# Kernel tuning notes

Hardware: AMD Instinct MI355X
Metric: run time of the kernel (lower is better)

The kernel has to match this reference:

```python
import jax, jax.numpy as jnp
import numpy as np

L, D, H, d = 16, 1024, 16, 64
NB, BS = 1024, 16        # num physical blocks, block size (tokens per block)
START_POS = 16368        # T = START_POS + L = 16384
SCALE = 1.0 / np.sqrt(d)


def setup_inputs() -> dict:
    key = jax.random.key(0)
    ks = jax.random.split(key, 5)
    return {
        "x": jax.random.normal(ks[0], (L, D), jnp.float32),
        "k_pool": jax.random.normal(ks[1], (NB, BS, H, d), jnp.float32),
        "v_pool": jax.random.normal(ks[2], (NB, BS, H, d), jnp.float32),
        "W_attn": jax.random.normal(ks[3], (D, 3 * D), jnp.float32) * 0.02,
        "b_attn": jnp.zeros((3 * D,), jnp.float32),
        "W_proj": jax.random.normal(ks[4], (D, D), jnp.float32) * 0.02,
        "b_proj": jnp.zeros((D,), jnp.float32),
        "block_ids": jnp.arange(NB, dtype=jnp.int64),
        "start_pos": START_POS,
    }


def reference(x, k_pool, v_pool, W_attn, b_attn, W_proj, b_proj, block_ids, start_pos):
    # QKV projection
    qkv = x @ W_attn + b_attn                      # [L, 3D]
    q, k, v = jnp.split(qkv, 3, axis=-1)
    q = q.reshape(L, H, d)
    k = k.reshape(L, H, d)
    v = v.reshape(L, H, d)

    # paged write of new K/V into the pool
    pos = start_pos + jnp.arange(L)                # logical positions of new tokens
    blk = block_ids[pos // BS]                     # physical block per token
    off = pos % BS
    k_pool = k_pool.at[blk, off].set(k)
    v_pool = v_pool.at[blk, off].set(v)

    # paged read of the full prefix [0, T)
    T = start_pos + L
    k_pos = jnp.arange(T)
    kb = block_ids[k_pos // BS]
    ko = k_pos % BS
    k_cache = k_pool[kb, ko]                       # [T, H, d]
    v_cache = v_pool[kb, ko]                       # [T, H, d]

    # attention: scores [H, L, T]
    scores = jnp.einsum("lhd,thd->hlt", q, k_cache) * SCALE
    mask = k_pos[None, :] > pos[:, None]           # [L, T] future positions
    scores = jnp.where(mask[None, :, :], -jnp.inf, scores)
    attn = jax.nn.softmax(scores.astype(jnp.float32), axis=-1).astype(scores.dtype)

    out = jnp.einsum("hlt,thd->lhd", attn, v_cache).reshape(L, D)
    return out @ W_proj + b_proj
```

## Files before the change

### kernel.cpp

```cpp
#include <hip/hip_runtime.h>
#include <math.h>

#define L_TOK 16
#define DMODEL 1024
#define NHEAD 16
#define DHEAD 64
#define NBLK 1024
#define BSZ 16
#define START_POS_C 16368
#define TTOT 16384
#define SPLITS 128
#define KSPLIT 16
#define QSCALE (0.125f * 1.4426950408889634f)

#define OFF_QKVP 0
#define OFF_QW   (OFF_QKVP + KSPLIT * L_TOK * 3 * DMODEL)
#define OFF_ACC  (OFF_QW + NHEAD * L_TOK * DHEAD)
#define OFF_M    (OFF_ACC + NHEAD * SPLITS * L_TOK * DHEAD)
#define OFF_SE   (OFF_M + NHEAD * SPLITS * L_TOK)
#define OFF_ATTN (OFF_SE + NHEAD * SPLITS * L_TOK)
#define OFF_PROJP (OFF_ATTN + L_TOK * DMODEL)
#define OFF_KNEW (OFF_PROJP + KSPLIT * L_TOK * DMODEL)
#define OFF_VNEW (OFF_KNEW + L_TOK * NHEAD * DHEAD)

typedef _Float16 half4_t __attribute__((ext_vector_type(4)));
typedef _Float16 half8_t __attribute__((ext_vector_type(8)));
typedef float float4v __attribute__((ext_vector_type(4)));

union H8 { _Float16 h[8]; half8_t v; };
union H4 { _Float16 h[4]; half4_t v; };

#define LDS_DMA16(gsrc, ldst)                                                        \
    __builtin_amdgcn_global_load_lds(                                                \
        (const __attribute__((address_space(1))) void*)(gsrc),                       \
        (__attribute__((address_space(3))) void*)(ldst), 16, 0, 0)

__device__ __forceinline__ void load_batch(float* buf, const float* Wp, int bk, int ncols) {
#pragma unroll
    for (int i = 0; i < 16; ++i) buf[i] = Wp[(size_t)(bk + i) * ncols];
}

__device__ __forceinline__ void fma_batch(float4v* acc_, const float* buf,
                                          const float* sxT, int bk) {
#pragma unroll
    for (int i = 0; i < 16; ++i) {
        const float wv_ = buf[i];
        const float4v* xp = (const float4v*)&sxT[(bk + i) * 20];
        float4v xa = xp[0], xb = xp[1], xc = xp[2], xd = xp[3];
        acc_[0] += xa * wv_;
        acc_[1] += xb * wv_;
        acc_[2] += xc * wv_;
        acc_[3] += xd * wv_;
    }
}

__global__ __launch_bounds__(256) void gemm_part(const float* __restrict__ x,
                                                 const float* __restrict__ W,
                                                 float* __restrict__ part,
                                                 int ncols) {
    const int col = blockIdx.x * 256 + threadIdx.x;
    const int k0 = blockIdx.y * (DMODEL / KSPLIT);

    __shared__ __align__(16) float sxT[64 * 20];
#pragma unroll
    for (int i = threadIdx.x; i < 64 * 16; i += 256) {
        int k = i & 63, l = i >> 6;
        sxT[k * 20 + l] = x[(size_t)l * DMODEL + k0 + k];
    }

    const float* Wp = W + (size_t)k0 * ncols + col;
    float wa[16], wb[16];
    load_batch(wa, Wp, 0, ncols);
    load_batch(wb, Wp, 16, ncols);
    __builtin_amdgcn_sched_barrier(0);
    __syncthreads();

    float4v acc_[4];
#pragma unroll
    for (int g = 0; g < 4; ++g) acc_[g] = (float4v){0.f, 0.f, 0.f, 0.f};

    fma_batch(acc_, wa, sxT, 0);
    load_batch(wa, Wp, 32, ncols);
    __builtin_amdgcn_sched_barrier(0);
    fma_batch(acc_, wb, sxT, 16);
    load_batch(wb, Wp, 48, ncols);
    __builtin_amdgcn_sched_barrier(0);
    fma_batch(acc_, wa, sxT, 32);
    fma_batch(acc_, wb, sxT, 48);

    const size_t base = ((size_t)blockIdx.y * L_TOK) * ncols + col;
#pragma unroll
    for (int g = 0; g < 4; ++g)
#pragma unroll
        for (int j = 0; j < 4; ++j)
            part[base + (size_t)(4 * g + j) * ncols] = acc_[g][j];
}

__global__ __launch_bounds__(256) void qkv_reduce_scatter(const float* __restrict__ part,
                                                          const float* __restrict__ b_attn,
                                                          float* __restrict__ qws,
                                                          float* __restrict__ knew,
                                                          float* __restrict__ vnew) {
    int tid = blockIdx.x * 256 + threadIdx.x;
    int n = tid % (3 * DMODEL);
    int l = tid / (3 * DMODEL);
    float p[KSPLIT];
#pragma unroll
    for (int kb = 0; kb < KSPLIT; ++kb)
        p[kb] = part[((size_t)kb * L_TOK + l) * (3 * DMODEL) + n];
    float s = b_attn[n];
#pragma unroll
    for (int st = 1; st < KSPLIT; st <<= 1)
#pragma unroll
        for (int i = 0; i < KSPLIT; i += 2 * st) p[i] += p[i + st];
    s += p[0];
    int sec = n >> 10;
    int m = n & (DMODEL - 1);
    int h = m >> 6;
    int dd = m & 63;
    if (sec == 0) {
        qws[(h * L_TOK + l) * DHEAD + dd] = s * QSCALE;
    } else {
        size_t idx = ((size_t)l * NHEAD + h) * DHEAD + dd;
        if (sec == 1) knew[idx] = s;
        else          vnew[idx] = s;
    }
}

__device__ __forceinline__ void stage_tile(const float* __restrict__ gk,
                                           const float* __restrict__ gv,
                                           float* kb, float* vb,
                                           int w, int lane, int hgrp) {
#pragma unroll
    for (int i = 0; i < 4; ++i) {
        const int tok = 4 * w + i;
        const int lx = lane ^ (tok & 7);
#pragma unroll
        for (int part = 0; part < 2; ++part) {
            const size_t go = (size_t)tok * 1024 + hgrp * 512 + part * 256 + lx * 4;
            LDS_DMA16(gk + go, kb + tok * 512 + part * 256);
            LDS_DMA16(gv + go, vb + tok * 512 + part * 256);
        }
    }
}

__device__ __forceinline__ void kv_base(const float* __restrict__ kpool,
                                        const float* __restrict__ vpool,
                                        const float* __restrict__ knew,
                                        const float* __restrict__ vnew,
                                        const int* blks, int s, int t,
                                        const float*& gk, const float*& gv) {
    if (s == SPLITS - 1 && t == 7) {
        gk = knew; gv = vnew;
    } else {
        gk = kpool + (size_t)blks[t] * 16384;
        gv = vpool + (size_t)blks[t] * 16384;
    }
}

__device__ __forceinline__ void attn_tile(const float* kt, const float* vt,
                                          int hh, half8_t qlo, half8_t qhi,
                                          float4v* acc, float& m_run, float& se_run,
                                          int tb, int c, int quad) {
    const int keyc = c & 7;
    const int hb = hh << 4;
    const float* krow = kt + c * 512;
    float4v a0 = *(const float4v*)&krow[(((hb | (2 * quad)) ^ keyc) << 2)];
    float4v a1 = *(const float4v*)&krow[(((hb | (2 * quad + 1)) ^ keyc) << 2)];
    float4v a2 = *(const float4v*)&krow[(((hb | (2 * quad + 8)) ^ keyc) << 2)];
    float4v a3 = *(const float4v*)&krow[(((hb | (2 * quad + 9)) ^ keyc) << 2)];
    H8 ka, kb;
    ka.h[0]=(_Float16)a0[0]; ka.h[1]=(_Float16)a0[1]; ka.h[2]=(_Float16)a0[2]; ka.h[3]=(_Float16)a0[3];
    ka.h[4]=(_Float16)a1[0]; ka.h[5]=(_Float16)a1[1]; ka.h[6]=(_Float16)a1[2]; ka.h[7]=(_Float16)a1[3];
    kb.h[0]=(_Float16)a2[0]; kb.h[1]=(_Float16)a2[1]; kb.h[2]=(_Float16)a2[2]; kb.h[3]=(_Float16)a2[3];
    kb.h[4]=(_Float16)a3[0]; kb.h[5]=(_Float16)a3[1]; kb.h[6]=(_Float16)a3[2]; kb.h[7]=(_Float16)a3[3];
    const float4v z4 = {0.f, 0.f, 0.f, 0.f};
    float4v st = __builtin_amdgcn_mfma_f32_16x16x32_f16(ka.v, qlo, z4, 0, 0, 0);
    st = __builtin_amdgcn_mfma_f32_16x16x32_f16(kb.v, qhi, st, 0, 0, 0);

    if (tb + 15 > START_POS_C) {
#pragma unroll
        for (int r = 0; r < 4; ++r)
            if (tb + 4 * quad + r > START_POS_C + c) st[r] = -INFINITY;
    }

    float tm = fmaxf(fmaxf(st[0], st[1]), fmaxf(st[2], st[3]));
    tm = fmaxf(tm, __shfl_xor(tm, 16, 64));
    tm = fmaxf(tm, __shfl_xor(tm, 32, 64));
    const float m_new = fmaxf(m_run, tm);
    const float fac = exp2f(m_run - m_new);
    H4 pa;
    pa.h[0]=(_Float16)exp2f(st[0]-m_new); pa.h[1]=(_Float16)exp2f(st[1]-m_new);
    pa.h[2]=(_Float16)exp2f(st[2]-m_new); pa.h[3]=(_Float16)exp2f(st[3]-m_new);
    float tsum = ((float)pa.h[0] + (float)pa.h[1]) + ((float)pa.h[2] + (float)pa.h[3]);
    tsum += __shfl_xor(tsum, 16, 64);
    tsum += __shfl_xor(tsum, 32, 64);
    se_run = se_run * fac + tsum;
    m_run = m_new;
    float4v fv;
    fv[0] = __shfl(fac, 4 * quad + 0, 64);
    fv[1] = __shfl(fac, 4 * quad + 1, 64);
    fv[2] = __shfl(fac, 4 * quad + 2, 64);
    fv[3] = __shfl(fac, 4 * quad + 3, 64);
#pragma unroll
    for (int ndv = 0; ndv < 4; ++ndv) acc[ndv] *= fv;
#pragma unroll
    for (int ndv = 0; ndv < 4; ++ndv) {
        H4 bf;
#pragma unroll
        for (int j = 0; j < 4; ++j) {
            const int tokr = 4 * quad + j;
            const int slot = (hb | (4 * ndv + (c >> 2))) ^ (tokr & 7);
            bf.h[j] = (_Float16)vt[tokr * 512 + (slot << 2) + (c & 3)];
        }
        acc[ndv] = __builtin_amdgcn_mfma_f32_16x16x16f16(pa.v, bf.v, acc[ndv], 0, 0, 0);
    }
}

__global__ __launch_bounds__(256, 1) void paged_attn(const float* __restrict__ kpool,
                                                     const float* __restrict__ vpool,
                                                     const int* __restrict__ block_ids,
                                                     const float* __restrict__ qws,
                                                     const float* __restrict__ knew,
                                                     const float* __restrict__ vnew,
                                                     float* __restrict__ accws,
                                                     float* __restrict__ m_arr,
                                                     float* __restrict__ se_arr) {
    const int hgrp = blockIdx.x;
    const int s = blockIdx.y;
    const int tid = threadIdx.x;
    const int w = tid >> 6;
    const int lane = tid & 63;
    const int c = lane & 15;
    const int quad = lane >> 4;

    __shared__ __align__(16) float kbuf[2][8192];
    __shared__ __align__(16) float vbuf[2][8192];

    int blks[8];
#pragma unroll
    for (int t = 0; t < 8; ++t) blks[t] = block_ids[s * 8 + t];

    const int h0 = hgrp * 8 + 2 * w;
    H8 qA0, qA1, qB0, qB1;
    {
        const float* qr = qws + ((size_t)(h0 * L_TOK + c)) * DHEAD + quad * 8;
        float4 x0 = *(const float4*)(qr),        x1 = *(const float4*)(qr + 4);
        float4 x2 = *(const float4*)(qr + 32),   x3 = *(const float4*)(qr + 36);
        float4 y0 = *(const float4*)(qr + 1024), y1 = *(const float4*)(qr + 1028);
        float4 y2 = *(const float4*)(qr + 1056), y3 = *(const float4*)(qr + 1060);
        qA0.h[0]=(_Float16)x0.x; qA0.h[1]=(_Float16)x0.y; qA0.h[2]=(_Float16)x0.z; qA0.h[3]=(_Float16)x0.w;
        qA0.h[4]=(_Float16)x1.x; qA0.h[5]=(_Float16)x1.y; qA0.h[6]=(_Float16)x1.z; qA0.h[7]=(_Float16)x1.w;
        qA1.h[0]=(_Float16)x2.x; qA1.h[1]=(_Float16)x2.y; qA1.h[2]=(_Float16)x2.z; qA1.h[3]=(_Float16)x2.w;
        qA1.h[4]=(_Float16)x3.x; qA1.h[5]=(_Float16)x3.y; qA1.h[6]=(_Float16)x3.z; qA1.h[7]=(_Float16)x3.w;
        qB0.h[0]=(_Float16)y0.x; qB0.h[1]=(_Float16)y0.y; qB0.h[2]=(_Float16)y0.z; qB0.h[3]=(_Float16)y0.w;
        qB0.h[4]=(_Float16)y1.x; qB0.h[5]=(_Float16)y1.y; qB0.h[6]=(_Float16)y1.z; qB0.h[7]=(_Float16)y1.w;
        qB1.h[0]=(_Float16)y2.x; qB1.h[1]=(_Float16)y2.y; qB1.h[2]=(_Float16)y2.z; qB1.h[3]=(_Float16)y2.w;
        qB1.h[4]=(_Float16)y3.x; qB1.h[5]=(_Float16)y3.y; qB1.h[6]=(_Float16)y3.z; qB1.h[7]=(_Float16)y3.w;
    }

    {
        const float* gk; const float* gv;
        kv_base(kpool, vpool, knew, vnew, blks, s, 0, gk, gv);
        stage_tile(gk, gv, kbuf[0], vbuf[0], w, lane, hgrp);
    }

    float4v accA[4], accB[4];
#pragma unroll
    for (int i = 0; i < 4; ++i) {
        accA[i] = (float4v){0.f, 0.f, 0.f, 0.f};
        accB[i] = (float4v){0.f, 0.f, 0.f, 0.f};
    }
    float mA = -INFINITY, seA = 0.f, mB = -INFINITY, seB = 0.f;

    float* kc = kbuf[0]; float* vc = vbuf[0];
    float* kn = kbuf[1]; float* vn = vbuf[1];

    for (int t = 0; t < 8; ++t) {
        if (t < 7) {
            const float* gk; const float* gv;
            kv_base(kpool, vpool, knew, vnew, blks, s, t + 1, gk, gv);
            stage_tile(gk, gv, kn, vn, w, lane, hgrp);
            asm volatile("s_waitcnt vmcnt(16)" ::: "memory");
        } else {
            asm volatile("s_waitcnt vmcnt(0)" ::: "memory");
        }
        __builtin_amdgcn_sched_barrier(0);
        __builtin_amdgcn_s_barrier();

        const int tb = s * 128 + t * 16;
        attn_tile(kc, vc, 2 * w,     qA0.v, qA1.v, accA, mA, seA, tb, c, quad);
        attn_tile(kc, vc, 2 * w + 1, qB0.v, qB1.v, accB, mB, seB, tb, c, quad);

        __builtin_amdgcn_s_barrier();
        float* tk = kc; kc = kn; kn = tk;
        float* tv = vc; vc = vn; vn = tv;
    }

    const size_t obA = ((size_t)(h0 * SPLITS + s) * L_TOK) * DHEAD;
    const size_t obB = ((size_t)((h0 + 1) * SPLITS + s) * L_TOK) * DHEAD;
#pragma unroll
    for (int ndv = 0; ndv < 4; ++ndv)
#pragma unroll
        for (int r = 0; r < 4; ++r) {
            accws[obA + (size_t)(4 * quad + r) * DHEAD + 16 * ndv + c] = accA[ndv][r];
            accws[obB + (size_t)(4 * quad + r) * DHEAD + 16 * ndv + c] = accB[ndv][r];
        }
    if (quad == 0) {
        const size_t mbA = (size_t)(h0 * SPLITS + s) * L_TOK + c;
        const size_t mbB = (size_t)((h0 + 1) * SPLITS + s) * L_TOK + c;
        m_arr[mbA] = mA; se_arr[mbA] = seA;
        m_arr[mbB] = mB; se_arr[mbB] = seB;
    }
}

__global__ __launch_bounds__(256) void combine(const float* __restrict__ accws,
                                               const float* __restrict__ m_arr,
                                               const float* __restrict__ se_arr,
                                               float* __restrict__ attnws) {
    const int h = blockIdx.x >> 4;
    const int l = blockIdx.x & 15;
    const int w = threadIdx.x >> 6;
    const int lane = threadIdx.x & 63;
    __shared__ float sm[4], sse[4], sacc[4][64];

    const size_t base = (size_t)h * SPLITS * L_TOK + l;

    float mreg[SPLITS / 4];
#pragma unroll
    for (int i = 0; i < SPLITS / 4; ++i)
        mreg[i] = m_arr[base + (size_t)(w + 4 * i) * L_TOK];
    float M = -INFINITY;
#pragma unroll
    for (int i = 0; i < SPLITS / 4; ++i) M = fmaxf(M, mreg[i]);

    float num = 0.f, den = 0.f;
#pragma unroll
    for (int i = 0; i < SPLITS / 4; ++i) {
        const size_t idx = base + (size_t)(w + 4 * i) * L_TOK;
        const float wgt = exp2f(mreg[i] - M);
        num = fmaf(wgt, accws[idx * DHEAD + lane], num);
        den = fmaf(wgt, se_arr[idx], den);
    }

    if (lane == 0) { sm[w] = M; sse[w] = den; }
    sacc[w][lane] = num;
    __syncthreads();
    if (w == 0) {
        const float M0 = fmaxf(fmaxf(sm[0], sm[1]), fmaxf(sm[2], sm[3]));
        float nn = 0.f, dd = 0.f;
#pragma unroll
        for (int i = 0; i < 4; ++i) {
            const float wgt = exp2f(sm[i] - M0);
            nn = fmaf(wgt, sacc[i][lane], nn);
            dd = fmaf(wgt, sse[i], dd);
        }
        attnws[(size_t)l * DMODEL + h * DHEAD + lane] = nn / dd;
    }
}

__global__ __launch_bounds__(256) void proj_reduce(const float* __restrict__ part,
                                                   const float* __restrict__ bias,
                                                   float* __restrict__ out) {
    int tid = blockIdx.x * 256 + threadIdx.x;
    int n = tid & (DMODEL - 1);
    int l = tid >> 10;
    float p[KSPLIT];
#pragma unroll
    for (int kb = 0; kb < KSPLIT; ++kb)
        p[kb] = part[((size_t)kb * L_TOK + l) * DMODEL + n];
#pragma unroll
    for (int st = 1; st < KSPLIT; st <<= 1)
#pragma unroll
        for (int i = 0; i < KSPLIT; i += 2 * st) p[i] += p[i + st];
    out[tid] = bias[n] + p[0];
}

extern "C" void kernel_launch(void* const* d_in, const int* in_sizes, int n_in,
                              void* d_out, int out_size, void* d_ws, size_t ws_size,
                              hipStream_t stream) {
    const float* x       = (const float*)d_in[0];
    const float* kpool   = (const float*)d_in[1];
    const float* vpool   = (const float*)d_in[2];
    const float* W_attn  = (const float*)d_in[3];
    const float* b_attn  = (const float*)d_in[4];
    const float* W_proj  = (const float*)d_in[5];
    const float* b_proj  = (const float*)d_in[6];
    const int* block_ids = (const int*)d_in[7];
    float* ws  = (float*)d_ws;
    float* out = (float*)d_out;

    gemm_part<<<dim3(12, KSPLIT), 256, 0, stream>>>(x, W_attn, ws + OFF_QKVP, 3 * DMODEL);
    qkv_reduce_scatter<<<192, 256, 0, stream>>>(ws + OFF_QKVP, b_attn,
                                                ws + OFF_QW, ws + OFF_KNEW, ws + OFF_VNEW);
    paged_attn<<<dim3(2, SPLITS), 256, 0, stream>>>(kpool, vpool, block_ids,
                                                    ws + OFF_QW, ws + OFF_KNEW, ws + OFF_VNEW,
                                                    ws + OFF_ACC, ws + OFF_M, ws + OFF_SE);
    combine<<<NHEAD * L_TOK, 256, 0, stream>>>(ws + OFF_ACC, ws + OFF_M, ws + OFF_SE,
                                               ws + OFF_ATTN);
    gemm_part<<<dim3(4, KSPLIT), 256, 0, stream>>>(ws + OFF_ATTN, W_proj, ws + OFF_PROJP, DMODEL);
    proj_reduce<<<64, 256, 0, stream>>>(ws + OFF_PROJP, b_proj, out);
}
```

Baseline: 199.2 us.

## Fuse all six stages into one cooperative persistent kernel with grid syncs

Merges the QKV GEMM, reduce/scatter, paged attention, combine, projection GEMM and final reduce into one cooperative kernel of 256 blocks, separated by grid-wide syncs. This removes five kernel launches and the gaps between them. In exchange every block reserves 128KB of LDS for all phases, and each grid sync costs something. The previous multi-kernel path stays as a fallback if the cooperative launch fails.

Result: slower. 351.7 us (+76.5%).

```diff
diff --git a/kernel.cpp b/kernel.cpp
--- a/kernel.cpp
+++ b/kernel.cpp
@@ -1,5 +1,8 @@
 #include <hip/hip_runtime.h>
+#include <hip/hip_cooperative_groups.h>
 #include <math.h>
+
+namespace cg = cooperative_groups;
 
 #define L_TOK 16
 #define DMODEL 1024
@@ -35,6 +38,7 @@
         (const __attribute__((address_space(1))) void*)(gsrc),                       \
         (__attribute__((address_space(3))) void*)(ldst), 16, 0, 0)
 
+
 __device__ __forceinline__ void load_batch(float* buf, const float* Wp, int bk, int ncols) {
 #pragma unroll
     for (int i = 0; i < 16; ++i) buf[i] = Wp[(size_t)(bk + i) * ncols];
@@ -54,31 +58,25 @@
     }
 }
 
-__global__ __launch_bounds__(256) void gemm_part(const float* __restrict__ x,
-                                                 const float* __restrict__ W,
-                                                 float* __restrict__ part,
-                                                 int ncols) {
-    const int col = blockIdx.x * 256 + threadIdx.x;
-    const int k0 = blockIdx.y * (DMODEL / KSPLIT);
-
-    __shared__ __align__(16) float sxT[64 * 20];
-#pragma unroll
-    for (int i = threadIdx.x; i < 64 * 16; i += 256) {
+__device__ __forceinline__ void gemm_body(const float* x, const float* W, float* part,
+                                          int ncols, int bx, int by, float* smem, int tid) {
+    const int col = bx * 256 + tid;
+    const int k0 = by * (DMODEL / KSPLIT);
+    float* sxT = smem;
+#pragma unroll
+    for (int i = tid; i < 64 * 16; i += 256) {
         int k = i & 63, l = i >> 6;
         sxT[k * 20 + l] = x[(size_t)l * DMODEL + k0 + k];
     }
-
     const float* Wp = W + (size_t)k0 * ncols + col;
     float wa[16], wb[16];
     load_batch(wa, Wp, 0, ncols);
     load_batch(wb, Wp, 16, ncols);
     __builtin_amdgcn_sched_barrier(0);
     __syncthreads();
-
     float4v acc_[4];
 #pragma unroll
     for (int g = 0; g < 4; ++g) acc_[g] = (float4v){0.f, 0.f, 0.f, 0.f};
-
     fma_batch(acc_, wa, sxT, 0);
     load_batch(wa, Wp, 32, ncols);
     __builtin_amdgcn_sched_barrier(0);
@@ -87,8 +85,7 @@
     __builtin_amdgcn_sched_barrier(0);
     fma_batch(acc_, wa, sxT, 32);
     fma_batch(acc_, wb, sxT, 48);
-
-    const size_t base = ((size_t)blockIdx.y * L_TOK) * ncols + col;
+    const size_t base = ((size_t)by * L_TOK) * ncols + col;
 #pragma unroll
     for (int g = 0; g < 4; ++g)
 #pragma unroll
@@ -96,14 +93,12 @@
             part[base + (size_t)(4 * g + j) * ncols] = acc_[g][j];
 }
 
-__global__ __launch_bounds__(256) void qkv_reduce_scatter(const float* __restrict__ part,
-                                                          const float* __restrict__ b_attn,
-                                                          float* __restrict__ qws,
-                                                          float* __restrict__ knew,
-                                                          float* __restrict__ vnew) {
-    int tid = blockIdx.x * 256 + threadIdx.x;
-    int n = tid % (3 * DMODEL);
-    int l = tid / (3 * DMODEL);
+__device__ __forceinline__ void qkv_reduce_body(const float* part, const float* b_attn,
+                                                float* qws, float* knew, float* vnew,
+                                                int b, int tid) {
+    int tg = b * 256 + tid;
+    int n = tg % (3 * DMODEL);
+    int l = tg / (3 * DMODEL);
     float p[KSPLIT];
 #pragma unroll
     for (int kb = 0; kb < KSPLIT; ++kb)
@@ -127,8 +122,7 @@
     }
 }
 
-__device__ __forceinline__ void stage_tile(const float* __restrict__ gk,
-                                           const float* __restrict__ gv,
+__device__ __forceinline__ void stage_tile(const float* gk, const float* gv,
                                            float* kb, float* vb,
                                            int w, int lane, int hgrp) {
 #pragma unroll
@@ -144,10 +138,8 @@
     }
 }
 
-__device__ __forceinline__ void kv_base(const float* __restrict__ kpool,
-                                        const float* __restrict__ vpool,
-                                        const float* __restrict__ knew,
-                                        const float* __restrict__ vnew,
+__device__ __forceinline__ void kv_base(const float* kpool, const float* vpool,
+                                        const float* knew, const float* vnew,
                                         const int* blks, int s, int t,
                                         const float*& gk, const float*& gv) {
     if (s == SPLITS - 1 && t == 7) {
@@ -217,25 +209,20 @@
     }
 }
 
-__global__ __launch_bounds__(256, 1) void paged_attn(const float* __restrict__ kpool,
-                                                     const float* __restrict__ vpool,
-                                                     const int* __restrict__ block_ids,
-                                                     const float* __restrict__ qws,
-                                                     const float* __restrict__ knew,
-                                                     const float* __restrict__ vnew,
-                                                     float* __restrict__ accws,
-                                                     float* __restrict__ m_arr,
-                                                     float* __restrict__ se_arr) {
-    const int hgrp = blockIdx.x;
-    const int s = blockIdx.y;
-    const int tid = threadIdx.x;
+__device__ __forceinline__ void attn_body(const float* kpool, const float* vpool,
+                                          const int* block_ids, const float* qws,
+                                          const float* knew, const float* vnew,
+                                          float* accws, float* m_arr, float* se_arr,
+                                          int hgrp, int s, int tid, float* smem) {
     const int w = tid >> 6;
     const int lane = tid & 63;
     const int c = lane & 15;
     const int quad = lane >> 4;
 
-    __shared__ __align__(16) float kbuf[2][8192];
-    __shared__ __align__(16) float vbuf[2][8192];
+    float* kb0 = smem;
+    float* kb1 = smem + 8192;
+    float* vb0 = smem + 16384;
+    float* vb1 = smem + 24576;
 
     int blks[8];
 #pragma unroll
@@ -262,7 +249,7 @@
     {
         const float* gk; const float* gv;
         kv_base(kpool, vpool, knew, vnew, blks, s, 0, gk, gv);
-        stage_tile(gk, gv, kbuf[0], vbuf[0], w, lane, hgrp);
+        stage_tile(gk, gv, kb0, vb0, w, lane, hgrp);
     }
 
     float4v accA[4], accB[4];
@@ -273,8 +260,8 @@
     }
     float mA = -INFINITY, seA = 0.f, mB = -INFINITY, seB = 0.f;
 
-    float* kc = kbuf[0]; float* vc = vbuf[0];
-    float* kn = kbuf[1]; float* vn = vbuf[1];
+    float* kc = kb0; float* vc = vb0;
+    float* kn = kb1; float* vn = vb1;
 
     for (int t = 0; t < 8; ++t) {
         if (t < 7) {
@@ -314,15 +301,14 @@
     }
 }
 
-__global__ __launch_bounds__(256) void combine(const float* __restrict__ accws,
-                                               const float* __restrict__ m_arr,
-                                               const float* __restrict__ se_arr,
-                                               float* __restrict__ attnws) {
-    const int h = blockIdx.x >> 4;
-    const int l = blockIdx.x & 15;
-    const int w = threadIdx.x >> 6;
-    const int lane = threadIdx.x & 63;
-    __shared__ float sm[4], sse[4], sacc[4][64];
+__device__ __forceinline__ void combine_body(const float* accws, const float* m_arr,
+                                             const float* se_arr, float* attnws,
+                                             int h, int l, int tid, float* smem) {
+    const int w = tid >> 6;
+    const int lane = tid & 63;
+    float* sm = smem;
+    float* sse = smem + 4;
+    float (*sacc)[64] = (float (*)[64])(smem + 8);
 
     const size_t base = (size_t)h * SPLITS * L_TOK + l;
 
@@ -359,12 +345,11 @@
     }
 }
 
-__global__ __launch_bounds__(256) void proj_reduce(const float* __restrict__ part,
-                                                   const float* __restrict__ bias,
-                                                   float* __restrict__ out) {
-    int tid = blockIdx.x * 256 + threadIdx.x;
-    int n = tid & (DMODEL - 1);
-    int l = tid >> 10;
+__device__ __forceinline__ void proj_reduce_body(const float* part, const float* bias,
+                                                 float* out, int b, int tid) {
+    int tg = b * 256 + tid;
+    int n = tg & (DMODEL - 1);
+    int l = tg >> 10;
     float p[KSPLIT];
 #pragma unroll
     for (int kb = 0; kb < KSPLIT; ++kb)
@@ -373,7 +358,85 @@
     for (int st = 1; st < KSPLIT; st <<= 1)
 #pragma unroll
         for (int i = 0; i < KSPLIT; i += 2 * st) p[i] += p[i + st];
-    out[tid] = bias[n] + p[0];
+    out[tg] = bias[n] + p[0];
+}
+
+__global__ __launch_bounds__(256, 1) void mega(const float* x, const float* kpool,
+                                               const float* vpool, const float* W_attn,
+                                               const float* b_attn, const float* W_proj,
+                                               const float* b_proj, const int* block_ids,
+                                               float* ws, float* out) {
+    cg::grid_group gg = cg::this_grid();
+    const int b = blockIdx.x;
+    const int tid = threadIdx.x;
+    __shared__ __align__(16) float smem[32768];
+
+    float* const qkvp   = ws + OFF_QKVP;
+    float* const qws    = ws + OFF_QW;
+    float* const accws  = ws + OFF_ACC;
+    float* const m_arr  = ws + OFF_M;
+    float* const se_arr = ws + OFF_SE;
+    float* const attnws = ws + OFF_ATTN;
+    float* const projp  = ws + OFF_PROJP;
+    float* const knew   = ws + OFF_KNEW;
+    float* const vnew   = ws + OFF_VNEW;
+
+    if (b < 192) gemm_body(x, W_attn, qkvp, 3 * DMODEL, b % 12, b / 12, smem, tid);
+    gg.sync();
+    if (b < 192) qkv_reduce_body(qkvp, b_attn, qws, knew, vnew, b, tid);
+    gg.sync();
+    attn_body(kpool, vpool, block_ids, qws, knew, vnew, accws, m_arr, se_arr,
+              b & 1, b >> 1, tid, smem);
+    gg.sync();
+    combine_body(accws, m_arr, se_arr, attnws, b >> 4, b & 15, tid, smem);
+    gg.sync();
+    if (b < 64) gemm_body(attnws, W_proj, projp, DMODEL, b % 4, b / 4, smem, tid);
+    gg.sync();
+    if (b < 64) proj_reduce_body(projp, b_proj, out, b, tid);
+}
+
+__global__ __launch_bounds__(256) void gemm_part_k(const float* __restrict__ x,
+                                                   const float* __restrict__ W,
+                                                   float* __restrict__ part, int ncols) {
+    __shared__ __align__(16) float sxT[64 * 20];
+    gemm_body(x, W, part, ncols, blockIdx.x, blockIdx.y, sxT, threadIdx.x);
+}
+
+__global__ __launch_bounds__(256) void qkv_reduce_k(const float* __restrict__ part,
+                                                    const float* __restrict__ b_attn,
+                                                    float* __restrict__ qws,
+                                                    float* __restrict__ knew,
+                                                    float* __restrict__ vnew) {
+    qkv_reduce_body(part, b_attn, qws, knew, vnew, blockIdx.x, threadIdx.x);
+}
+
+__global__ __launch_bounds__(256, 1) void paged_attn_k(const float* __restrict__ kpool,
+                                                       const float* __restrict__ vpool,
+                                                       const int* __restrict__ block_ids,
+                                                       const float* __restrict__ qws,
+                                                       const float* __restrict__ knew,
+                                                       const float* __restrict__ vnew,
+                                                       float* __restrict__ accws,
+                                                       float* __restrict__ m_arr,
+                                                       float* __restrict__ se_arr) {
+    __shared__ __align__(16) float smem[32768];
+    attn_body(kpool, vpool, block_ids, qws, knew, vnew, accws, m_arr, se_arr,
+              blockIdx.x, blockIdx.y, threadIdx.x, smem);
+}
+
+__global__ __launch_bounds__(256) void combine_k(const float* __restrict__ accws,
+                                                 const float* __restrict__ m_arr,
+                                                 const float* __restrict__ se_arr,
+                                                 float* __restrict__ attnws) {
+    __shared__ float smem[264];
+    combine_body(accws, m_arr, se_arr, attnws, blockIdx.x >> 4, blockIdx.x & 15,
+                 threadIdx.x, smem);
+}
+
+__global__ __launch_bounds__(256) void proj_reduce_k(const float* __restrict__ part,
+                                                     const float* __restrict__ bias,
+                                                     float* __restrict__ out) {
+    proj_reduce_body(part, bias, out, blockIdx.x, threadIdx.x);
 }
 
 extern "C" void kernel_launch(void* const* d_in, const int* in_sizes, int n_in,
@@ -390,14 +453,23 @@
     float* ws  = (float*)d_ws;
     float* out = (float*)d_out;
 
-    gemm_part<<<dim3(12, KSPLIT), 256, 0, stream>>>(x, W_attn, ws + OFF_QKVP, 3 * DMODEL);
-    qkv_reduce_scatter<<<192, 256, 0, stream>>>(ws + OFF_QKVP, b_attn,
-                                                ws + OFF_QW, ws + OFF_KNEW, ws + OFF_VNEW);
-    paged_attn<<<dim3(2, SPLITS), 256, 0, stream>>>(kpool, vpool, block_ids,
-                                                    ws + OFF_QW, ws + OFF_KNEW, ws + OFF_VNEW,
-                                                    ws + OFF_ACC, ws + OFF_M, ws + OFF_SE);
-    combine<<<NHEAD * L_TOK, 256, 0, stream>>>(ws + OFF_ACC, ws + OFF_M, ws + OFF_SE,
-                                               ws + OFF_ATTN);
-    gemm_part<<<dim3(4, KSPLIT), 256, 0, stream>>>(ws + OFF_ATTN, W_proj, ws + OFF_PROJP, DMODEL);
-    proj_reduce<<<64, 256, 0, stream>>>(ws + OFF_PROJP, b_proj, out);
-}
+    void* args[] = { (void*)&x, (void*)&kpool, (void*)&vpool, (void*)&W_attn,
+                     (void*)&b_attn, (void*)&W_proj, (void*)&b_proj,
+                     (void*)&block_ids, (void*)&ws, (void*)&out };
+    hipError_t err = hipLaunchCooperativeKernel((const void*)mega, dim3(256), dim3(256),
+                                                args, 0, stream);
+    if (err != hipSuccess) {
+        gemm_part_k<<<dim3(12, KSPLIT), 256, 0, stream>>>(x, W_attn, ws + OFF_QKVP, 3 * DMODEL);
+        qkv_reduce_k<<<192, 256, 0, stream>>>(ws + OFF_QKVP, b_attn,
+                                              ws + OFF_QW, ws + OFF_KNEW, ws + OFF_VNEW);
+        paged_attn_k<<<dim3(2, SPLITS), 256, 0, stream>>>(kpool, vpool, block_ids,
+                                                          ws + OFF_QW, ws + OFF_KNEW,
+                                                          ws + OFF_VNEW, ws + OFF_ACC,
+                                                          ws + OFF_M, ws + OFF_SE);
+        combine_k<<<NHEAD * L_TOK, 256, 0, stream>>>(ws + OFF_ACC, ws + OFF_M, ws + OFF_SE,
+                                                     ws + OFF_ATTN);
+        gemm_part_k<<<dim3(4, KSPLIT), 256, 0, stream>>>(ws + OFF_ATTN, W_proj,
+                                                         ws + OFF_PROJP, DMODEL);
+        proj_reduce_k<<<64, 256, 0, stream>>>(ws + OFF_PROJP, b_proj, out);
+    }
+}
```
